# Kernel optimization log

Measured on AMD Instinct MI355X. Metric: run time of the kernel, lower is better.

Reference implementation:

```python
import jax, jax.numpy as jnp
import numpy as np

N, D, H, E, C = 10000, 256, 512, 320000, 1  # nodes, feature_dim, nhid, edges, nclass


def setup_inputs() -> dict:
    key = jax.random.key(0)
    ks = jax.random.split(key, 8)
    x = jax.random.normal(ks[0], (N, D), jnp.float32)
    edge_src = jax.random.randint(ks[1], (E,), 0, N, jnp.int32)
    edge_dst = jax.random.randint(ks[2], (E,), 0, N, jnp.int32)
    # adjacency values of a row-normalized A (mean aggregation); ~1/avg_degree scale
    edge_val = jax.random.uniform(ks[3], (E,), jnp.float32) / 32.0
    W_conv = jax.random.normal(ks[4], (2 * D, H), jnp.float32) / np.sqrt(2 * D)
    b_conv = jnp.zeros((H,), jnp.float32)
    W1 = jax.random.normal(ks[5], (H, H), jnp.float32) / np.sqrt(H)
    b1 = jnp.zeros((H,), jnp.float32)
    prelu_a = jnp.full((H,), 0.25, jnp.float32)  # PReLU per-channel slope (torch init 0.25)
    W2 = jax.random.normal(ks[6], (H, C), jnp.float32) / np.sqrt(H)
    b2 = jnp.zeros((C,), jnp.float32)
    return dict(x=x, edge_src=edge_src, edge_dst=edge_dst, edge_val=edge_val,
                W_conv=W_conv, b_conv=b_conv, W1=W1, b1=b1,
                prelu_a=prelu_a, W2=W2, b2=b2)


def reference(x, edge_src, edge_dst, edge_val, W_conv, b_conv, W1, b1, prelu_a, W2, b2):
    # MeanAggregator: agg = spmm(A, x) with A given as (dst, src, val) edge list
    msgs = x[edge_src] * edge_val[:, None]                         # [E, D] gather + scale
    agg = jax.ops.segment_sum(msgs, edge_dst, num_segments=x.shape[0])  # [N, D]
    # GraphConv: concat(self, agg) -> linear -> ReLU
    cat = jnp.concatenate([x, agg], axis=-1)                       # [N, 2D]
    h = jax.nn.relu(cat @ W_conv + b_conv)                         # [N, H]
    # classifier: Linear -> PReLU -> Linear, then view(-1)
    z = h @ W1 + b1                                                # [N, H]
    z = jnp.where(z > 0, z, prelu_a * z)                           # PReLU(nhid)
    pred = (z @ W2 + b2).reshape(-1)                               # [N * nclass]
    return pred
```

## Files before the change

### kernel.cpp

```cpp
#include <hip/hip_runtime.h>
#include <hip/hip_bf16.h>

#define N_NODES 10000
#define M_PAD   10112
#define DIM     256
#define HID     512
#define KDIM    512
#define N_EDGE  320000
#define ELL_W   128

typedef __attribute__((ext_vector_type(4))) float  f32x4;
typedef __attribute__((ext_vector_type(8))) __bf16 bf16x8;

__device__ __forceinline__ unsigned short f2bf(float f) {
    union { float f; unsigned int u; } v; v.f = f;
    unsigned int r = v.u + 0x7FFFu + ((v.u >> 16) & 1u);
    return (unsigned short)(r >> 16);
}
__device__ __forceinline__ float bf2f(unsigned short u) {
    union { unsigned int i; float f; } v; v.i = ((unsigned int)u) << 16;
    return v.f;
}

__global__ void k_zero(int* __restrict__ deg) {
    int i = blockIdx.x * 256 + threadIdx.x;
    if (i < 10240) deg[i] = 0;
}

__global__ void k_prep(const int* __restrict__ esrc, const int* __restrict__ edst,
                       const float* __restrict__ eval,
                       int* __restrict__ deg, int2* __restrict__ ell,
                       const float* __restrict__ x, unsigned short* __restrict__ cat,
                       const float* __restrict__ Wc, unsigned short* __restrict__ Wct,
                       const float* __restrict__ W1, unsigned short* __restrict__ W1t) {
    int b = blockIdx.x;
    if (b < 1250) {
        int e = b * 256 + threadIdx.x;
        if (e < N_EDGE) {
            int d = edst[e];
            int slot = atomicAdd(&deg[d], 1);
            if (slot < ELL_W)
                ell[(size_t)d * ELL_W + slot] = make_int2(esrc[e], __float_as_int(eval[e]));
        }
    } else if (b < 3750) {
        int t  = (b - 1250) * 256 + threadIdx.x;
        int n  = t >> 6;
        int c4 = (t & 63) * 4;
        f32x4 v = *(const f32x4*)(x + (size_t)n * DIM + c4);
        ushort4 o;
        o.x = f2bf(v.x); o.y = f2bf(v.y); o.z = f2bf(v.z); o.w = f2bf(v.w);
        *(ushort4*)(cat + (size_t)n * 2 * DIM + c4) = o;
    } else if (b < 4774) {
        int t = (b - 3750) * 256 + threadIdx.x;
        int k = t >> 9, n = t & 511;
        Wct[(size_t)n * 512 + k] = f2bf(Wc[(size_t)k * 512 + n]);
    } else {
        int t = (b - 4774) * 256 + threadIdx.x;
        int k = t >> 9, n = t & 511;
        W1t[(size_t)n * 512 + k] = f2bf(W1[(size_t)k * 512 + n]);
    }
}

__global__ void k_agg(const int* __restrict__ deg, const int2* __restrict__ ell,
                      unsigned short* __restrict__ cat) {
    int wid  = (blockIdx.x * blockDim.x + threadIdx.x) >> 6;
    int lane = threadIdx.x & 63;
    if (wid >= N_NODES) return;
    int cnt = deg[wid];
    if (cnt > ELL_W) cnt = ELL_W;
    const int2* row = ell + (size_t)wid * ELL_W;
    int c4 = lane * 4;
    f32x4 a0 = {0.f,0.f,0.f,0.f}, a1 = a0, a2 = a0, a3 = a0;
    for (int base = 0; base < cnt; base += 64) {
        int m = cnt - base;
        if (m > 64) m = 64;
        int2 my = make_int2(0, 0);
        if (lane < m) my = row[base + lane];
        int j = 0;
        for (; j + 4 <= m; j += 4) {
            int   s0 = __builtin_amdgcn_readlane(my.x, j);
            float v0 = __int_as_float(__builtin_amdgcn_readlane(my.y, j));
            int   s1 = __builtin_amdgcn_readlane(my.x, j + 1);
            float v1 = __int_as_float(__builtin_amdgcn_readlane(my.y, j + 1));
            int   s2 = __builtin_amdgcn_readlane(my.x, j + 2);
            float v2 = __int_as_float(__builtin_amdgcn_readlane(my.y, j + 2));
            int   s3 = __builtin_amdgcn_readlane(my.x, j + 3);
            float v3 = __int_as_float(__builtin_amdgcn_readlane(my.y, j + 3));
            ushort4 q0 = *(const ushort4*)(cat + (size_t)s0 * 2 * DIM + c4);
            ushort4 q1 = *(const ushort4*)(cat + (size_t)s1 * 2 * DIM + c4);
            ushort4 q2 = *(const ushort4*)(cat + (size_t)s2 * 2 * DIM + c4);
            ushort4 q3 = *(const ushort4*)(cat + (size_t)s3 * 2 * DIM + c4);
            a0.x += v0 * bf2f(q0.x); a0.y += v0 * bf2f(q0.y);
            a0.z += v0 * bf2f(q0.z); a0.w += v0 * bf2f(q0.w);
            a1.x += v1 * bf2f(q1.x); a1.y += v1 * bf2f(q1.y);
            a1.z += v1 * bf2f(q1.z); a1.w += v1 * bf2f(q1.w);
            a2.x += v2 * bf2f(q2.x); a2.y += v2 * bf2f(q2.y);
            a2.z += v2 * bf2f(q2.z); a2.w += v2 * bf2f(q2.w);
            a3.x += v3 * bf2f(q3.x); a3.y += v3 * bf2f(q3.y);
            a3.z += v3 * bf2f(q3.z); a3.w += v3 * bf2f(q3.w);
        }
        for (; j < m; ++j) {
            int   s0 = __builtin_amdgcn_readlane(my.x, j);
            float v0 = __int_as_float(__builtin_amdgcn_readlane(my.y, j));
            ushort4 q0 = *(const ushort4*)(cat + (size_t)s0 * 2 * DIM + c4);
            a0.x += v0 * bf2f(q0.x); a0.y += v0 * bf2f(q0.y);
            a0.z += v0 * bf2f(q0.z); a0.w += v0 * bf2f(q0.w);
        }
    }
    ushort4 o;
    o.x = f2bf((a0.x + a1.x) + (a2.x + a3.x));
    o.y = f2bf((a0.y + a1.y) + (a2.y + a3.y));
    o.z = f2bf((a0.z + a1.z) + (a2.z + a3.z));
    o.w = f2bf((a0.w + a1.w) + (a2.w + a3.w));
    *(ushort4*)(cat + (size_t)wid * 2 * DIM + DIM + c4) = o;
}

#define LDSW 72

#define LOAD4(dst, p) { dst[0] = *(const f32x4*)(p); dst[1] = *(const f32x4*)((p) + 8); \
                        dst[2] = *(const f32x4*)((p) + 16); dst[3] = *(const f32x4*)((p) + 24); }
#define STORE4(p, src) { *(f32x4*)(p) = src[0]; *(f32x4*)((p) + 8) = src[1]; \
                         *(f32x4*)((p) + 16) = src[2]; *(f32x4*)((p) + 24) = src[3]; }

template <int MODE>
__global__ __launch_bounds__(256)
void k_gemm128(const unsigned short* __restrict__ A,
               const unsigned short* __restrict__ Bt,
               const float* __restrict__ bias,
               const float* __restrict__ pa,
               const float* __restrict__ w2,
               unsigned short* __restrict__ hout,
               float* __restrict__ part) {
    __shared__ unsigned short As[2][128 * LDSW];
    __shared__ unsigned short Bs[2][128 * LDSW];

    const int t    = threadIdx.x;
    const int lane = t & 63;
    const int w    = t >> 6;
    const int wr   = w >> 1, wc = w & 1;
    const int tn   = blockIdx.x & 3;
    const int tm   = blockIdx.x >> 2;
    const int gm0  = tm * 128, gn0 = tn * 128;

    const int srow = t >> 1;
    const int scol = (t & 1) * 32;
    const unsigned short* gA = A  + (size_t)(gm0 + srow) * KDIM + scol;
    const unsigned short* gB = Bt + (size_t)(gn0 + srow) * KDIM + scol;
    const int woff = srow * LDSW + scol;

    const int r15 = lane & 15;
    const int kf  = (lane >> 4) * 8;

    f32x4 acc[4][4] = {};
    f32x4 va[4], vb[4];

    LOAD4(va, gA);
    LOAD4(vb, gB);
    STORE4(&As[0][woff], va);
    STORE4(&Bs[0][woff], vb);
    __syncthreads();

    #pragma unroll
    for (int ks = 0; ks < 8; ++ks) {
        const int cur = ks & 1;
        if (ks < 7) {
            gA += 64; gB += 64;
            LOAD4(va, gA);
            LOAD4(vb, gB);
        }
        #pragma unroll
        for (int kk = 0; kk < 2; ++kk) {
            bf16x8 af[4], bf[4];
            #pragma unroll
            for (int m = 0; m < 4; ++m)
                af[m] = *(const bf16x8*)&As[cur][(wr * 64 + m * 16 + r15) * LDSW + kk * 32 + kf];
            #pragma unroll
            for (int n = 0; n < 4; ++n)
                bf[n] = *(const bf16x8*)&Bs[cur][(wc * 64 + n * 16 + r15) * LDSW + kk * 32 + kf];
            #pragma unroll
            for (int m = 0; m < 4; ++m)
                #pragma unroll
                for (int n = 0; n < 4; ++n)
                    acc[m][n] = __builtin_amdgcn_mfma_f32_16x16x32_bf16(af[m], bf[n], acc[m][n], 0, 0, 0);
        }
        if (ks < 7) {
            STORE4(&As[cur ^ 1][woff], va);
            STORE4(&Bs[cur ^ 1][woff], vb);
            __syncthreads();
        }
    }

    const int rq = lane >> 4;
    if (MODE == 0) {
        #pragma unroll
        for (int n = 0; n < 4; ++n) {
            int c = gn0 + wc * 64 + n * 16 + r15;
            float b = bias[c];
            #pragma unroll
            for (int m = 0; m < 4; ++m) {
                #pragma unroll
                for (int i = 0; i < 4; ++i) {
                    int row = gm0 + wr * 64 + m * 16 + rq * 4 + i;
                    float v = acc[m][n][i] + b;
                    v = v > 0.f ? v : 0.f;
                    hout[(size_t)row * HID + c] = f2bf(v);
                }
            }
        }
    } else {
        float rsum[4][4] = {};
        #pragma unroll
        for (int n = 0; n < 4; ++n) {
            int c = gn0 + wc * 64 + n * 16 + r15;
            float b = bias[c];
            float a = pa[c];
            float wv = w2[c];
            #pragma unroll
            for (int m = 0; m < 4; ++m)
                #pragma unroll
                for (int i = 0; i < 4; ++i) {
                    float v = acc[m][n][i] + b;
                    v = v > 0.f ? v : a * v;
                    rsum[m][i] += v * wv;
                }
        }
        #pragma unroll
        for (int m = 0; m < 4; ++m)
            #pragma unroll
            for (int i = 0; i < 4; ++i) {
                float s = rsum[m][i];
                s += __shfl_xor(s, 1);
                s += __shfl_xor(s, 2);
                s += __shfl_xor(s, 4);
                s += __shfl_xor(s, 8);
                if (r15 == 0) {
                    int row = gm0 + wr * 64 + m * 16 + rq * 4 + i;
                    part[(size_t)(tn * 2 + wc) * M_PAD + row] = s;
                }
            }
    }
}

__global__ void k_vout(const float* __restrict__ part, const float* __restrict__ b2,
                       float* __restrict__ pred) {
    int row = blockIdx.x * blockDim.x + threadIdx.x;
    if (row >= N_NODES) return;
    float s = b2[0];
    #pragma unroll
    for (int j = 0; j < 8; ++j) s += part[(size_t)j * M_PAD + row];
    pred[row] = s;
}

extern "C" void kernel_launch(void* const* d_in, const int* in_sizes, int n_in,
                              void* d_out, int out_size, void* d_ws, size_t ws_size,
                              hipStream_t stream) {
    const float* x    = (const float*)d_in[0];
    const int*   esrc = (const int*)  d_in[1];
    const int*   edst = (const int*)  d_in[2];
    const float* eval = (const float*)d_in[3];
    const float* Wc   = (const float*)d_in[4];
    const float* bc   = (const float*)d_in[5];
    const float* W1   = (const float*)d_in[6];
    const float* b1   = (const float*)d_in[7];
    const float* pa   = (const float*)d_in[8];
    const float* W2   = (const float*)d_in[9];
    const float* b2   = (const float*)d_in[10];
    float* pred = (float*)d_out;

    char* w = (char*)d_ws;
    int*            deg   = (int*)w;
    int2*           ell   = (int2*)(w + 40960);
    unsigned short* cat   = (unsigned short*)(w + 10526720);
    unsigned short* Wct   = (unsigned short*)(w + 20881408);
    unsigned short* W1t   = (unsigned short*)(w + 21405696);
    unsigned short* h     = (unsigned short*)(w + 21929984);
    float*          partb = (float*)(w + 32284672);

    k_zero<<<40, 256, 0, stream>>>(deg);

    k_prep<<<5798, 256, 0, stream>>>(esrc, edst, eval, deg, ell, x, cat, Wc, Wct, W1, W1t);

    k_agg<<<(N_NODES * 64 + 255) / 256, 256, 0, stream>>>(deg, ell, cat);

    k_gemm128<0><<<316, 256, 0, stream>>>(cat, Wct, bc, nullptr, nullptr, h, nullptr);
    k_gemm128<1><<<316, 256, 0, stream>>>(h, W1t, b1, pa, W2, nullptr, partb);

    k_vout<<<(N_NODES + 255) / 256, 256, 0, stream>>>(partb, b2, pred);
}
```

Before: 85.40 us.

## Deepen GEMM register prefetch, add XCD-aware tile swizzle, unroll aggregation by eight

The bf16 GEMM now keeps two register staging sets, so global loads for a K-tile are issued two iterations before they are written to LDS. This gives the global-load latency more time to hide behind the MFMA work. Blocks are remapped so that each XCD gets a contiguous range of output tiles, which should improve L2 reuse of the A and B panels. The sparse aggregation loop is unrolled to eight gathers with eight accumulators to put more loads in flight, at the cost of more VGPRs and possibly lower occupancy in both kernels.

```diff
diff --git a/kernel.cpp b/kernel.cpp
--- a/kernel.cpp
+++ b/kernel.cpp
@@ -71,13 +71,14 @@
     const int2* row = ell + (size_t)wid * ELL_W;
     int c4 = lane * 4;
     f32x4 a0 = {0.f,0.f,0.f,0.f}, a1 = a0, a2 = a0, a3 = a0;
+    f32x4 a4 = a0, a5 = a0, a6 = a0, a7 = a0;
     for (int base = 0; base < cnt; base += 64) {
         int m = cnt - base;
         if (m > 64) m = 64;
         int2 my = make_int2(0, 0);
         if (lane < m) my = row[base + lane];
         int j = 0;
-        for (; j + 4 <= m; j += 4) {
+        for (; j + 8 <= m; j += 8) {
             int   s0 = __builtin_amdgcn_readlane(my.x, j);
             float v0 = __int_as_float(__builtin_amdgcn_readlane(my.y, j));
             int   s1 = __builtin_amdgcn_readlane(my.x, j + 1);
@@ -86,10 +87,22 @@
             float v2 = __int_as_float(__builtin_amdgcn_readlane(my.y, j + 2));
             int   s3 = __builtin_amdgcn_readlane(my.x, j + 3);
             float v3 = __int_as_float(__builtin_amdgcn_readlane(my.y, j + 3));
+            int   s4 = __builtin_amdgcn_readlane(my.x, j + 4);
+            float v4 = __int_as_float(__builtin_amdgcn_readlane(my.y, j + 4));
+            int   s5 = __builtin_amdgcn_readlane(my.x, j + 5);
+            float v5 = __int_as_float(__builtin_amdgcn_readlane(my.y, j + 5));
+            int   s6 = __builtin_amdgcn_readlane(my.x, j + 6);
+            float v6 = __int_as_float(__builtin_amdgcn_readlane(my.y, j + 6));
+            int   s7 = __builtin_amdgcn_readlane(my.x, j + 7);
+            float v7 = __int_as_float(__builtin_amdgcn_readlane(my.y, j + 7));
             ushort4 q0 = *(const ushort4*)(cat + (size_t)s0 * 2 * DIM + c4);
             ushort4 q1 = *(const ushort4*)(cat + (size_t)s1 * 2 * DIM + c4);
             ushort4 q2 = *(const ushort4*)(cat + (size_t)s2 * 2 * DIM + c4);
             ushort4 q3 = *(const ushort4*)(cat + (size_t)s3 * 2 * DIM + c4);
+            ushort4 q4 = *(const ushort4*)(cat + (size_t)s4 * 2 * DIM + c4);
+            ushort4 q5 = *(const ushort4*)(cat + (size_t)s5 * 2 * DIM + c4);
+            ushort4 q6 = *(const ushort4*)(cat + (size_t)s6 * 2 * DIM + c4);
+            ushort4 q7 = *(const ushort4*)(cat + (size_t)s7 * 2 * DIM + c4);
             a0.x += v0 * bf2f(q0.x); a0.y += v0 * bf2f(q0.y);
             a0.z += v0 * bf2f(q0.z); a0.w += v0 * bf2f(q0.w);
             a1.x += v1 * bf2f(q1.x); a1.y += v1 * bf2f(q1.y);
@@ -98,6 +111,14 @@
             a2.z += v2 * bf2f(q2.z); a2.w += v2 * bf2f(q2.w);
             a3.x += v3 * bf2f(q3.x); a3.y += v3 * bf2f(q3.y);
             a3.z += v3 * bf2f(q3.z); a3.w += v3 * bf2f(q3.w);
+            a4.x += v4 * bf2f(q4.x); a4.y += v4 * bf2f(q4.y);
+            a4.z += v4 * bf2f(q4.z); a4.w += v4 * bf2f(q4.w);
+            a5.x += v5 * bf2f(q5.x); a5.y += v5 * bf2f(q5.y);
+            a5.z += v5 * bf2f(q5.z); a5.w += v5 * bf2f(q5.w);
+            a6.x += v6 * bf2f(q6.x); a6.y += v6 * bf2f(q6.y);
+            a6.z += v6 * bf2f(q6.z); a6.w += v6 * bf2f(q6.w);
+            a7.x += v7 * bf2f(q7.x); a7.y += v7 * bf2f(q7.y);
+            a7.z += v7 * bf2f(q7.z); a7.w += v7 * bf2f(q7.w);
         }
         for (; j < m; ++j) {
             int   s0 = __builtin_amdgcn_readlane(my.x, j);
@@ -108,19 +129,24 @@
         }
     }
     ushort4 o;
-    o.x = f2bf((a0.x + a1.x) + (a2.x + a3.x));
-    o.y = f2bf((a0.y + a1.y) + (a2.y + a3.y));
-    o.z = f2bf((a0.z + a1.z) + (a2.z + a3.z));
-    o.w = f2bf((a0.w + a1.w) + (a2.w + a3.w));
+    o.x = f2bf(((a0.x + a1.x) + (a2.x + a3.x)) + ((a4.x + a5.x) + (a6.x + a7.x)));
+    o.y = f2bf(((a0.y + a1.y) + (a2.y + a3.y)) + ((a4.y + a5.y) + (a6.y + a7.y)));
+    o.z = f2bf(((a0.z + a1.z) + (a2.z + a3.z)) + ((a4.z + a5.z) + (a6.z + a7.z)));
+    o.w = f2bf(((a0.w + a1.w) + (a2.w + a3.w)) + ((a4.w + a5.w) + (a6.w + a7.w)));
     *(ushort4*)(cat + (size_t)wid * 2 * DIM + DIM + c4) = o;
 }
 
 #define LDSW 72
 
-#define LOAD4(dst, p) { dst[0] = *(const f32x4*)(p); dst[1] = *(const f32x4*)((p) + 8); \
-                        dst[2] = *(const f32x4*)((p) + 16); dst[3] = *(const f32x4*)((p) + 24); }
-#define STORE4(p, src) { *(f32x4*)(p) = src[0]; *(f32x4*)((p) + 8) = src[1]; \
-                         *(f32x4*)((p) + 16) = src[2]; *(f32x4*)((p) + 24) = src[3]; }
+#define LOADT(s) { va[s][0] = *(const f32x4*)(gA);      va[s][1] = *(const f32x4*)(gA + 8); \
+                   va[s][2] = *(const f32x4*)(gA + 16); va[s][3] = *(const f32x4*)(gA + 24); \
+                   vb[s][0] = *(const f32x4*)(gB);      vb[s][1] = *(const f32x4*)(gB + 8); \
+                   vb[s][2] = *(const f32x4*)(gB + 16); vb[s][3] = *(const f32x4*)(gB + 24); }
+#define STORET(buf, s) { \
+    *(f32x4*)&As[buf][woff]      = va[s][0]; *(f32x4*)&As[buf][woff + 8]  = va[s][1]; \
+    *(f32x4*)&As[buf][woff + 16] = va[s][2]; *(f32x4*)&As[buf][woff + 24] = va[s][3]; \
+    *(f32x4*)&Bs[buf][woff]      = vb[s][0]; *(f32x4*)&Bs[buf][woff + 8]  = vb[s][1]; \
+    *(f32x4*)&Bs[buf][woff + 16] = vb[s][2]; *(f32x4*)&Bs[buf][woff + 24] = vb[s][3]; }
 
 template <int MODE>
 __global__ __launch_bounds__(256)
@@ -138,8 +164,12 @@
     const int lane = t & 63;
     const int w    = t >> 6;
     const int wr   = w >> 1, wc = w & 1;
-    const int tn   = blockIdx.x & 3;
-    const int tm   = blockIdx.x >> 2;
+
+    const int orig = blockIdx.x;
+    const int xcd  = orig & 7, loc = orig >> 3;
+    const int swz  = (xcd < 4 ? xcd * 40 : 160 + (xcd - 4) * 39) + loc;
+    const int tn   = swz & 3;
+    const int tm   = swz >> 2;
     const int gm0  = tm * 128, gn0 = tn * 128;
 
     const int srow = t >> 1;
@@ -152,21 +182,20 @@
     const int kf  = (lane >> 4) * 8;
 
     f32x4 acc[4][4] = {};
-    f32x4 va[4], vb[4];
-
-    LOAD4(va, gA);
-    LOAD4(vb, gB);
-    STORE4(&As[0][woff], va);
-    STORE4(&Bs[0][woff], vb);
+    f32x4 va[2][4], vb[2][4];
+
+    LOADT(0);
+    STORET(0, 0);
+    gA += 64; gB += 64;
+    LOADT(1);
     __syncthreads();
 
     #pragma unroll
     for (int ks = 0; ks < 8; ++ks) {
         const int cur = ks & 1;
-        if (ks < 7) {
+        if (ks < 6) {
             gA += 64; gB += 64;
-            LOAD4(va, gA);
-            LOAD4(vb, gB);
+            LOADT(cur);
         }
         #pragma unroll
         for (int kk = 0; kk < 2; ++kk) {
@@ -184,8 +213,7 @@
                     acc[m][n] = __builtin_amdgcn_mfma_f32_16x16x32_bf16(af[m], bf[n], acc[m][n], 0, 0, 0);
         }
         if (ks < 7) {
-            STORE4(&As[cur ^ 1][woff], va);
-            STORE4(&Bs[cur ^ 1][woff], vb);
+            STORET(cur ^ 1, (ks + 1) & 1);
             __syncthreads();
         }
     }
```

Result: slower. 90.84 us (+6.4%).

## Load A fragments directly from global into registers, skipping LDS staging

Applied to the files above, without the earlier changes.

The GEMM kernel no longer stages the A tile through shared memory. Each wave loads its MFMA A fragments straight from global memory into a double-buffered register array, prefetching the next k-step while the current one computes. This removes the LDS writes and reads for A and halves shared-memory use, which could raise occupancy. In exchange the two column-waves of each row load the same A rows redundantly, the global reads are less coalesced (16-byte per-lane row accesses), and register pressure rises.

```diff
diff --git a/kernel.cpp b/kernel.cpp
--- a/kernel.cpp
+++ b/kernel.cpp
@@ -117,10 +117,16 @@
 
 #define LDSW 72
 
-#define LOAD4(dst, p) { dst[0] = *(const f32x4*)(p); dst[1] = *(const f32x4*)((p) + 8); \
-                        dst[2] = *(const f32x4*)((p) + 16); dst[3] = *(const f32x4*)((p) + 24); }
-#define STORE4(p, src) { *(f32x4*)(p) = src[0]; *(f32x4*)((p) + 8) = src[1]; \
-                         *(f32x4*)((p) + 16) = src[2]; *(f32x4*)((p) + 24) = src[3]; }
+#define LOADB() { vb[0] = *(const f32x4*)(gB);      vb[1] = *(const f32x4*)(gB + 8); \
+                  vb[2] = *(const f32x4*)(gB + 16); vb[3] = *(const f32x4*)(gB + 24); }
+#define STOREB(buf) { \
+    *(f32x4*)&Bs[buf][woff]      = vb[0]; *(f32x4*)&Bs[buf][woff + 8]  = vb[1]; \
+    *(f32x4*)&Bs[buf][woff + 16] = vb[2]; *(f32x4*)&Bs[buf][woff + 24] = vb[3]; }
+#define LOADA(s, ks) { \
+    _Pragma("unroll") \
+    for (int m = 0; m < 4; ++m) { \
+        af[s][m]     = *(const bf16x8*)(ap[m] + (ks) * 64); \
+        af[s][4 + m] = *(const bf16x8*)(ap[m] + (ks) * 64 + 32); } }
 
 template <int MODE>
 __global__ __launch_bounds__(256)
@@ -131,7 +137,6 @@
                const float* __restrict__ w2,
                unsigned short* __restrict__ hout,
                float* __restrict__ part) {
-    __shared__ unsigned short As[2][128 * LDSW];
     __shared__ unsigned short Bs[2][128 * LDSW];
 
     const int t    = threadIdx.x;
@@ -144,36 +149,37 @@
 
     const int srow = t >> 1;
     const int scol = (t & 1) * 32;
-    const unsigned short* gA = A  + (size_t)(gm0 + srow) * KDIM + scol;
     const unsigned short* gB = Bt + (size_t)(gn0 + srow) * KDIM + scol;
     const int woff = srow * LDSW + scol;
 
     const int r15 = lane & 15;
     const int kf  = (lane >> 4) * 8;
 
+    const unsigned short* ap[4];
+    #pragma unroll
+    for (int m = 0; m < 4; ++m)
+        ap[m] = A + (size_t)(gm0 + wr * 64 + m * 16 + r15) * KDIM + kf;
+
     f32x4 acc[4][4] = {};
-    f32x4 va[4], vb[4];
-
-    LOAD4(va, gA);
-    LOAD4(vb, gB);
-    STORE4(&As[0][woff], va);
-    STORE4(&Bs[0][woff], vb);
+    f32x4 vb[4];
+    bf16x8 af[2][8];
+
+    LOADB();
+    STOREB(0);
+    LOADA(0, 0);
     __syncthreads();
 
     #pragma unroll
     for (int ks = 0; ks < 8; ++ks) {
         const int cur = ks & 1;
         if (ks < 7) {
-            gA += 64; gB += 64;
-            LOAD4(va, gA);
-            LOAD4(vb, gB);
+            gB += 64;
+            LOADB();
+            LOADA(cur ^ 1, ks + 1);
         }
         #pragma unroll
         for (int kk = 0; kk < 2; ++kk) {
-            bf16x8 af[4], bf[4];
-            #pragma unroll
-            for (int m = 0; m < 4; ++m)
-                af[m] = *(const bf16x8*)&As[cur][(wr * 64 + m * 16 + r15) * LDSW + kk * 32 + kf];
+            bf16x8 bf[4];
             #pragma unroll
             for (int n = 0; n < 4; ++n)
                 bf[n] = *(const bf16x8*)&Bs[cur][(wc * 64 + n * 16 + r15) * LDSW + kk * 32 + kf];
@@ -181,11 +187,10 @@
             for (int m = 0; m < 4; ++m)
                 #pragma unroll
                 for (int n = 0; n < 4; ++n)
-                    acc[m][n] = __builtin_amdgcn_mfma_f32_16x16x32_bf16(af[m], bf[n], acc[m][n], 0, 0, 0);
+                    acc[m][n] = __builtin_amdgcn_mfma_f32_16x16x32_bf16(af[cur][kk * 4 + m], bf[n], acc[m][n], 0, 0, 0);
         }
         if (ks < 7) {
-            STORE4(&As[cur ^ 1][woff], va);
-            STORE4(&Bs[cur ^ 1][woff], vb);
+            STOREB(cur ^ 1);
             __syncthreads();
         }
     }
```

Result: slower. 101.4 us (+18.7%).
